# Kernel tuning notes

Hardware: AMD Instinct MI355X
Metric: run time of the kernel (lower is better)

## Reference

```python
import jax, jax.numpy as jnp
import numpy as np

H = 512

def _lstm_layer(x_tbd, W_ih, b, W_hh):
    # x_tbd: [T, B, D]; W_ih: [4H, D]; b: [4H]; W_hh: [4H, H]
    T, B, _ = x_tbd.shape
    # precompute input projections for all timesteps (same math, batched GEMM)
    xp = jnp.einsum('tbd,gd->tbg', x_tbd, W_ih) + b  # [T, B, 4H]

    def step(carry, xp_t):
        h, c = carry
        gates = xp_t + h @ W_hh.T  # [B, 4H]
        i, f, g, o = jnp.split(gates, 4, axis=-1)
        i = jax.nn.sigmoid(i)
        f = jax.nn.sigmoid(f)
        g = jnp.tanh(g)
        o = jax.nn.sigmoid(o)
        c_next = f * c + i * g
        h_next = o * jnp.tanh(c_next)
        return (h_next, c_next), h_next

    h0 = jnp.zeros((B, H), dtype=x_tbd.dtype)
    c0 = jnp.zeros((B, H), dtype=x_tbd.dtype)
    (h_n, c_n), hs = jax.lax.scan(step, (h0, c0), xp)
    return hs, h_n, c_n  # hs: [T, B, H]


def setup_inputs() -> dict:
    key = jax.random.key(0)
    ks = jax.random.split(key, 5)
    D = 256
    x = jax.random.normal(ks[0], (32, 1024, D), dtype=jnp.float32)
    s = 0.05
    W_ih0 = jax.random.normal(ks[1], (4 * H, D), dtype=jnp.float32) * s
    W_hh0 = jax.random.normal(ks[2], (4 * H, H), dtype=jnp.float32) * s
    W_ih1 = jax.random.normal(ks[3], (4 * H, H), dtype=jnp.float32) * s
    W_hh1 = jax.random.normal(ks[4], (4 * H, H), dtype=jnp.float32) * s
    # bias init: zeros, forget-gate slice [H:2H] = 1.0 (per _init_weights)
    b = jnp.zeros((4 * H,), dtype=jnp.float32).at[H:2 * H].set(1.0)
    return {"x": x, "W_ih0": W_ih0, "b0": b, "W_hh0": W_hh0,
            "W_ih1": W_ih1, "b1": b, "W_hh1": W_hh1}


def reference(x, W_ih0, b0, W_hh0, W_ih1, b1, W_hh1):
    # batch_first: [B, T, D] -> [T, B, D]
    x_tbd = jnp.transpose(x, (1, 0, 2))
    hs0, h0n, c0n = _lstm_layer(x_tbd, W_ih0, b0, W_hh0)
    hs1, h1n, c1n = _lstm_layer(hs0, W_ih1, b1, W_hh1)
    output = jnp.transpose(hs1, (1, 0, 2))  # [B, T, H]
    h_n = jnp.stack([h0n, h1n], axis=0)  # [num_layers, B, H]
    c_n = jnp.stack([c0n, c1n], axis=0)
    return output, h_n, c_n
```

## Files before the change

kernel.cpp:

```cpp
#include <hip/hip_runtime.h>


typedef __bf16 bf16x8 __attribute__((ext_vector_type(8)));
typedef float  f32x4  __attribute__((ext_vector_type(4)));
typedef float  f32x2  __attribute__((ext_vector_type(2)));
typedef unsigned long long u64;
typedef unsigned int u32;

#define MFMA16(a, b, c) __builtin_amdgcn_mfma_f32_16x16x32_bf16((a), (b), (c), 0, 0, 0)
#define SCOPE_AGENT __HIP_MEMORY_SCOPE_AGENT

__device__ __forceinline__ float fsigm(float x) { return 1.0f / (1.0f + __expf(-x)); }
__device__ __forceinline__ float ftanh(float x) {
    x = fminf(15.0f, fmaxf(-15.0f, x));
    float e = __expf(2.0f * x);
    return (e - 1.0f) / (e + 1.0f);
}

__device__ __forceinline__ bf16x8 frag_from(u64 lo, u64 hi) {
    union { u64 u[2]; bf16x8 v; } x;
    x.u[0] = lo; x.u[1] = hi;
    return x.v;
}

__global__ void pack_w3(const float* __restrict__ W0, const float* __restrict__ W1,
                        const float* __restrict__ W2, __bf16* __restrict__ O0,
                        __bf16* __restrict__ O1, __bf16* __restrict__ O2) {
    int gtid = blockIdx.x * 256 + threadIdx.x;
    int sel  = gtid >> 17;
    const float* W = (sel == 0) ? W0 : (sel == 1) ? W1 : W2;
    __bf16* WB     = (sel == 0) ? O0 : (sel == 1) ? O1 : O2;
    int tid  = gtid & 131071;
    int lane = tid & 63;
    int kk   = (tid >> 6) & 15;
    int v    = (tid >> 10) & 3;
    int w    = tid >> 12;
    int n    = v * 16 + (lane & 15);
    int grow = (n >> 4) * 512 + w * 16 + (n & 15);
    int k0   = kk * 32 + (lane >> 4) * 8;
    const float* src = W + (size_t)grow * 512 + k0;
    bf16x8 val;
#pragma unroll
    for (int e = 0; e < 8; e++) val[e] = (__bf16)src[e];
    *(bf16x8*)(WB + (size_t)tid * 8) = val;
}

__global__ __launch_bounds__(256, 2) void gemm_xp(const float* __restrict__ A,
                                                  const float* __restrict__ W,
                                                  __bf16* __restrict__ out, int K) {
    const int tid = threadIdx.x, lane = tid & 63, wv = tid >> 6;
    const int bm = blockIdx.x >> 4, bn = blockIdx.x & 15;
    const int m_base = bm * 128 + (wv & 1) * 64;
    const int n_base = bn * 128 + (wv >> 1) * 64;
    const int kq = (lane >> 4) * 8;
    const int rl = lane & 15;

    f32x4 acc[4][4];
#pragma unroll
    for (int i = 0; i < 4; i++)
#pragma unroll
        for (int j = 0; j < 4; j++) acc[i][j] = (f32x4){0.f, 0.f, 0.f, 0.f};

    const int nk = K >> 5;
    for (int kk = 0; kk < nk; kk++) {
        int k0 = kk * 32 + kq;
        bf16x8 af[4], bfr[4];
#pragma unroll
        for (int mt = 0; mt < 4; mt++) {
            int row = m_base + mt * 16 + rl;
            const float* ap = A + (size_t)((row & 31) * 1024 + (row >> 5)) * K + k0;
#pragma unroll
            for (int e = 0; e < 8; e++) af[mt][e] = (__bf16)ap[e];
        }
#pragma unroll
        for (int nt = 0; nt < 4; nt++) {
            int n = n_base + nt * 16 + rl;
            const float* wp = W + (size_t)n * K + k0;
#pragma unroll
            for (int e = 0; e < 8; e++) bfr[nt][e] = (__bf16)wp[e];
        }
#pragma unroll
        for (int mt = 0; mt < 4; mt++)
#pragma unroll
            for (int nt = 0; nt < 4; nt++)
                acc[mt][nt] = MFMA16(af[mt], bfr[nt], acc[mt][nt]);
    }

    const int rq = (lane >> 4) * 4;
#pragma unroll
    for (int mt = 0; mt < 4; mt++)
#pragma unroll
        for (int nt = 0; nt < 4; nt++)
#pragma unroll
            for (int r = 0; r < 4; r++) {
                int row = m_base + mt * 16 + rq + r;
                int col = n_base + nt * 16 + rl;
                out[(size_t)row * 2048 + col] = (__bf16)acc[mt][nt][r];
            }
}

__global__ __launch_bounds__(256, 1) void lstm_pipe3(
    const __bf16* __restrict__ xp0,
    const __bf16* __restrict__ WB0,
    const __bf16* __restrict__ WBw1,
    const __bf16* __restrict__ WBi1,
    const float* __restrict__ bias0,
    const float* __restrict__ bias1,
    __bf16* __restrict__ hbuf0,
    __bf16* __restrict__ hbuf1,
    __bf16* __restrict__ hs0s,
    __bf16* __restrict__ xp1r,
    float* __restrict__ out_f32,
    float* __restrict__ hn_out,
    float* __restrict__ cn_out,
    int* __restrict__ fL0,
    int* __restrict__ fX,
    int* __restrict__ fL1) {
    const int tid  = threadIdx.x;
    const int role = blockIdx.x >> 5;
    const int w    = blockIdx.x & 31;
    const int lane = tid & 63;
    const int wv   = tid >> 6;

    __shared__ __bf16 h_lds[32 * 516];
    __shared__ float  g_lds[32 * 68];

    bf16x8 wreg[16];
    {
        const __bf16* WB = (role == 0) ? WB0 : (role == 1) ? WBi1 : WBw1;
        const __bf16* wb = WB + (size_t)(w * 4 + wv) * 16 * 512 + lane * 8;
#pragma unroll
        for (int kk = 0; kk < 16; kk++) wreg[kk] = *(const bf16x8*)(wb + kk * 512);
    }

    const int b  = tid >> 3;
    const int jp = tid & 7;
    const int j0 = w * 16 + jp * 2;
    const int arow = lane & 15;
    const int kq8  = (lane >> 4) * 8;

    f32x2 bsv[4];
    if (role != 1) {
        const float* bias = (role == 0) ? bias0 : bias1;
#pragma unroll
        for (int g = 0; g < 4; g++) bsv[g] = *(const f32x2*)(bias + g * 512 + j0);
    }
    float cc0 = 0.f, cc1 = 0.f;

    __bf16* hbuf = (role == 0) ? hbuf0 : hbuf1;
    int* fMy = (role == 0) ? fL0 : (role == 1) ? fX : fL1;

    u32 xc[4] = {0, 0, 0, 0}, xn[4] = {0, 0, 0, 0};
    if (role == 0) {
#pragma unroll
        for (int g = 0; g < 4; g++)
            xc[g] = *(const u32*)(xp0 + (size_t)b * 2048 + g * 512 + j0);
    }

    for (int t = 0; t < 1024; t++) {
        if (role == 0) {
            int tn = (t < 1023) ? t + 1 : 1023;
#pragma unroll
            for (int g = 0; g < 4; g++)
                xn[g] = *(const u32*)(xp0 + (size_t)(tn * 32 + b) * 2048 + g * 512 + j0);
            if (t > 0) {
                if (tid < 32)
                    while (__hip_atomic_load(&fL0[tid * 1024 + t - 1], __ATOMIC_RELAXED,
                                             SCOPE_AGENT) == 0) {}
                asm volatile("" ::: "memory");
                __syncthreads();
            }
        } else if (role == 1) {
            if (tid < 32)
                while (__hip_atomic_load(&fL0[tid * 1024 + t], __ATOMIC_RELAXED,
                                         SCOPE_AGENT) == 0) {}
            else if (tid == 32 && t >= 4)
                while (__hip_atomic_load(&fL1[w * 1024 + t - 4], __ATOMIC_RELAXED,
                                         SCOPE_AGENT) == 0) {}
            asm volatile("" ::: "memory");
            __syncthreads();
        } else {
            if (tid < 32) {
                if (t > 0)
                    while (__hip_atomic_load(&fL1[tid * 1024 + t - 1], __ATOMIC_RELAXED,
                                             SCOPE_AGENT) == 0) {}
            } else if (tid == 32) {
                while (__hip_atomic_load(&fX[w * 1024 + t], __ATOMIC_RELAXED,
                                         SCOPE_AGENT) == 0) {}
            }
            asm volatile("" ::: "memory");
            __syncthreads();
        }

        u32 xpr[4];
        if (role == 2) {
            const __bf16* xs = xp1r + (size_t)(t & 3) * 65536 + (size_t)b * 2048 + j0;
#pragma unroll
            for (int g = 0; g < 4; g++)
                xpr[g] = __hip_atomic_load((const u32*)(xs + g * 512),
                                           __ATOMIC_RELAXED, SCOPE_AGENT);
        }
        {
            const u64* hg = (role == 1)
                ? (const u64*)(hs0s + (size_t)t * 16384)
                : (const u64*)(hbuf + (size_t)(t & 1) * 16384);
            u64 hv[16];
#pragma unroll
            for (int i = 0; i < 16; i++)
                hv[i] = __hip_atomic_load(hg + i * 256 + tid, __ATOMIC_RELAXED, SCOPE_AGENT);
#pragma unroll
            for (int i = 0; i < 16; i++) {
                int f  = (i * 256 + tid) * 4;
                int br = f >> 9, col = f & 511;
                *(u64*)(h_lds + br * 516 + col) = hv[i];
            }
        }
        __syncthreads();

        f32x4 acc0 = (f32x4){0.f, 0.f, 0.f, 0.f};
        f32x4 acc1 = (f32x4){0.f, 0.f, 0.f, 0.f};
#pragma unroll
        for (int kk = 0; kk < 16; kk++) {
            const __bf16* p0 = h_lds + arow * 516 + kq8 + kk * 32;
            const __bf16* p1 = p0 + 16 * 516;
            bf16x8 a0 = frag_from(*(const u64*)p0, *(const u64*)(p0 + 4));
            bf16x8 a1 = frag_from(*(const u64*)p1, *(const u64*)(p1 + 4));
            acc0 = MFMA16(a0, wreg[kk], acc0);
            acc1 = MFMA16(a1, wreg[kk], acc1);
        }
        {
            int col   = wv * 16 + (lane & 15);
            int rbase = (lane >> 4) * 4;
#pragma unroll
            for (int r = 0; r < 4; r++) {
                g_lds[(rbase + r) * 68 + col]      = acc0[r];
                g_lds[(16 + rbase + r) * 68 + col] = acc1[r];
            }
        }
        __syncthreads();

        if (role == 1) {
            const float* gl = g_lds + b * 68 + jp * 2;
            __bf16* xd = xp1r + (size_t)(t & 3) * 65536 + (size_t)b * 2048 + j0;
#pragma unroll
            for (int g = 0; g < 4; g++) {
                f32x2 gv = *(const f32x2*)(gl + g * 16);
                union { __bf16 v2[2]; u32 u; } pu;
                pu.v2[0] = (__bf16)gv[0]; pu.v2[1] = (__bf16)gv[1];
                __hip_atomic_store((u32*)(xd + g * 512), pu.u,
                                   __ATOMIC_RELAXED, SCOPE_AGENT);
            }
            asm volatile("s_waitcnt vmcnt(0)" ::: "memory");
            __syncthreads();
            if (tid == 0)
                __hip_atomic_store(&fX[w * 1024 + t], 1, __ATOMIC_RELAXED, SCOPE_AGENT);
        } else {
            float hf0, hf1;
            {
                u32 x0 = (role == 0) ? xc[0] : xpr[0];
                u32 x1 = (role == 0) ? xc[1] : xpr[1];
                u32 x2 = (role == 0) ? xc[2] : xpr[2];
                u32 x3 = (role == 0) ? xc[3] : xpr[3];
                union { u32 u; __bf16 v2[2]; } xi, xf, xg, xo;
                xi.u = x0; xf.u = x1; xg.u = x2; xo.u = x3;
                const float* gl = g_lds + b * 68 + jp * 2;
                f32x2 gi = *(const f32x2*)(gl);
                f32x2 gf = *(const f32x2*)(gl + 16);
                f32x2 gg = *(const f32x2*)(gl + 32);
                f32x2 go = *(const f32x2*)(gl + 48);

                float i0 = fsigm(gi[0] + (float)xi.v2[0] + bsv[0][0]);
                float f0 = fsigm(gf[0] + (float)xf.v2[0] + bsv[1][0]);
                float g0 = ftanh(gg[0] + (float)xg.v2[0] + bsv[2][0]);
                float o0 = fsigm(go[0] + (float)xo.v2[0] + bsv[3][0]);
                cc0 = f0 * cc0 + i0 * g0;
                hf0 = o0 * ftanh(cc0);

                float i1 = fsigm(gi[1] + (float)xi.v2[1] + bsv[0][1]);
                float f1 = fsigm(gf[1] + (float)xf.v2[1] + bsv[1][1]);
                float g1 = ftanh(gg[1] + (float)xg.v2[1] + bsv[2][1]);
                float o1 = fsigm(go[1] + (float)xo.v2[1] + bsv[3][1]);
                cc1 = f1 * cc1 + i1 * g1;
                hf1 = o1 * ftanh(cc1);
            }
            union { __bf16 v2[2]; u32 u; } hu;
            hu.v2[0] = (__bf16)hf0; hu.v2[1] = (__bf16)hf1;

            __hip_atomic_store((u32*)(hbuf + (size_t)((t + 1) & 1) * 16384 +
                                      (size_t)b * 512 + j0),
                               hu.u, __ATOMIC_RELAXED, SCOPE_AGENT);
            if (role == 0)
                __hip_atomic_store((u32*)(hs0s + ((size_t)t * 32 + b) * 512 + j0), hu.u,
                                   __ATOMIC_RELAXED, SCOPE_AGENT);
            asm volatile("s_waitcnt vmcnt(0)" ::: "memory");
            __syncthreads();
            if (tid == 0)
                __hip_atomic_store(&fMy[w * 1024 + t], 1, __ATOMIC_RELAXED, SCOPE_AGENT);

            if (role == 2)
                *(f32x2*)(out_f32 + (size_t)b * 524288 + (size_t)t * 512 + j0) =
                    (f32x2){hf0, hf1};
            if (t == 1023) {
                int li = (role == 0) ? 0 : 1;
                *(f32x2*)(hn_out + (size_t)li * 16384 + (size_t)b * 512 + j0) =
                    (f32x2){hf0, hf1};
                *(f32x2*)(cn_out + (size_t)li * 16384 + (size_t)b * 512 + j0) =
                    (f32x2){cc0, cc1};
            }
#pragma unroll
            for (int g = 0; g < 4; g++) xc[g] = xn[g];
        }
    }
}

extern "C" void kernel_launch(void* const* d_in, const int* in_sizes, int n_in,
                              void* d_out, int out_size, void* d_ws, size_t ws_size,
                              hipStream_t stream) {
    (void)in_sizes; (void)n_in; (void)out_size; (void)ws_size;
    const float* x    = (const float*)d_in[0];
    const float* Wih0 = (const float*)d_in[1];
    const float* b0   = (const float*)d_in[2];
    const float* Whh0 = (const float*)d_in[3];
    const float* Wih1 = (const float*)d_in[4];
    const float* b1   = (const float*)d_in[5];
    const float* Whh1 = (const float*)d_in[6];
    float* dout = (float*)d_out;

    char* wsb = (char*)d_ws;
    int*    fL0   = (int*)wsb;
    int*    fX    = (int*)(wsb + (128 << 10));
    int*    fL1   = (int*)(wsb + (256 << 10));
    __bf16* hbuf0 = (__bf16*)(wsb + (384 << 10));
    __bf16* hbuf1 = (__bf16*)(wsb + (448 << 10));
    __bf16* WB0   = (__bf16*)(wsb + (512 << 10));
    __bf16* WBw1  = (__bf16*)(wsb + (512 << 10) + (2 << 20));
    __bf16* WBi1  = (__bf16*)(wsb + (512 << 10) + (4 << 20));
    __bf16* xp1r  = (__bf16*)(wsb + (512 << 10) + (6 << 20));
    __bf16* hs0s  = (__bf16*)(wsb + (1 << 20) + (7 << 20));
    __bf16* xpb   = (__bf16*)(wsb + (40 << 20));

    (void)hipMemsetAsync(wsb, 0, 512 << 10, stream);

    pack_w3<<<dim3(1536), dim3(256), 0, stream>>>(Whh0, Whh1, Wih1, WB0, WBw1, WBi1);

    gemm_xp<<<dim3(4096), dim3(256), 0, stream>>>(x, Wih0, xpb, 256);

    lstm_pipe3<<<dim3(96), dim3(256), 0, stream>>>(
        xpb, WB0, WBw1, WBi1, b0, b1, hbuf0, hbuf1, hs0s, xp1r,
        dout, dout + 16777216, dout + 16777216 + 32768, fL0, fX, fL1);
}
```

Baseline: 3.869 ms.

## Embed phase tags in recurrent h buffers to replace flag-based step sync

The recurrent hidden-state exchange now stores each bf16 pair alongside a 32-bit phase tag in a 64-bit word. Consumers poll the data directly until every tag matches the expected phase, instead of waiting on per-block flags. This removes the store-drain wait, barrier and flag write from the critical path of layer 0's and layer 1's recurrences. In exchange, the h buffers double in size, every poll reads twice as many bytes, and readers spin on the payload itself. Layer 1 now signals its flag (used for throttling the xp1 ring) at step start rather than after writing h.

Result: slower. 4.030 ms (+4.2%).

```diff
diff --git a/kernel.cpp b/kernel.cpp
--- a/kernel.cpp
+++ b/kernel.cpp
@@ -21,6 +21,26 @@
     union { u64 u[2]; bf16x8 v; } x;
     x.u[0] = lo; x.u[1] = hi;
     return x.v;
+}
+
+__device__ __forceinline__ void poll_pairs16(const u64* __restrict__ base, int tid,
+                                             u32 ph, u64* hv) {
+    u64 q0[16], q1[16];
+    u32 bad;
+    do {
+#pragma unroll
+        for (int i = 0; i < 16; i++) {
+            int f = i * 256 + tid;
+            q0[i] = __hip_atomic_load(base + 2 * f,     __ATOMIC_RELAXED, SCOPE_AGENT);
+            q1[i] = __hip_atomic_load(base + 2 * f + 1, __ATOMIC_RELAXED, SCOPE_AGENT);
+        }
+        bad = 0;
+#pragma unroll
+        for (int i = 0; i < 16; i++)
+            bad |= ((u32)(q0[i] >> 32) ^ ph) | ((u32)(q1[i] >> 32) ^ ph);
+    } while (bad != 0);
+#pragma unroll
+    for (int i = 0; i < 16; i++) hv[i] = (q0[i] & 0xFFFFFFFFull) | (q1[i] << 32);
 }
 
 __global__ void pack_w3(const float* __restrict__ W0, const float* __restrict__ W1,
@@ -106,8 +126,8 @@
     const __bf16* __restrict__ WBi1,
     const float* __restrict__ bias0,
     const float* __restrict__ bias1,
-    __bf16* __restrict__ hbuf0,
-    __bf16* __restrict__ hbuf1,
+    u64* __restrict__ hbuf0,
+    u64* __restrict__ hbuf1,
     __bf16* __restrict__ hs0s,
     __bf16* __restrict__ xp1r,
     float* __restrict__ out_f32,
@@ -136,6 +156,7 @@
     const int b  = tid >> 3;
     const int jp = tid & 7;
     const int j0 = w * 16 + jp * 2;
+    const int pi = b * 256 + w * 8 + jp;
     const int arow = lane & 15;
     const int kq8  = (lane >> 4) * 8;
 
@@ -147,8 +168,7 @@
     }
     float cc0 = 0.f, cc1 = 0.f;
 
-    __bf16* hbuf = (role == 0) ? hbuf0 : hbuf1;
-    int* fMy = (role == 0) ? fL0 : (role == 1) ? fX : fL1;
+    u64* hbuf = (role == 0) ? hbuf0 : hbuf1;
 
     u32 xc[4] = {0, 0, 0, 0}, xn[4] = {0, 0, 0, 0};
     if (role == 0) {
@@ -158,17 +178,19 @@
     }
 
     for (int t = 0; t < 1024; t++) {
+        u64 hv[16];
+        u32 xpr[4];
+
         if (role == 0) {
             int tn = (t < 1023) ? t + 1 : 1023;
 #pragma unroll
             for (int g = 0; g < 4; g++)
                 xn[g] = *(const u32*)(xp0 + (size_t)(tn * 32 + b) * 2048 + g * 512 + j0);
             if (t > 0) {
-                if (tid < 32)
-                    while (__hip_atomic_load(&fL0[tid * 1024 + t - 1], __ATOMIC_RELAXED,
-                                             SCOPE_AGENT) == 0) {}
-                asm volatile("" ::: "memory");
-                __syncthreads();
+                poll_pairs16(hbuf0 + (size_t)(t & 1) * 8192, tid, (u32)(t >> 1) + 1, hv);
+            } else {
+#pragma unroll
+                for (int i = 0; i < 16; i++) hv[i] = 0;
             }
         } else if (role == 1) {
             if (tid < 32)
@@ -179,43 +201,40 @@
                                          SCOPE_AGENT) == 0) {}
             asm volatile("" ::: "memory");
             __syncthreads();
+            const u64* hg = (const u64*)(hs0s + (size_t)t * 16384);
+#pragma unroll
+            for (int i = 0; i < 16; i++)
+                hv[i] = __hip_atomic_load(hg + i * 256 + tid, __ATOMIC_RELAXED, SCOPE_AGENT);
         } else {
-            if (tid < 32) {
-                if (t > 0)
-                    while (__hip_atomic_load(&fL1[tid * 1024 + t - 1], __ATOMIC_RELAXED,
-                                             SCOPE_AGENT) == 0) {}
-            } else if (tid == 32) {
+            if (tid == 32)
                 while (__hip_atomic_load(&fX[w * 1024 + t], __ATOMIC_RELAXED,
                                          SCOPE_AGENT) == 0) {}
-            }
             asm volatile("" ::: "memory");
             __syncthreads();
-        }
-
-        u32 xpr[4];
-        if (role == 2) {
             const __bf16* xs = xp1r + (size_t)(t & 3) * 65536 + (size_t)b * 2048 + j0;
 #pragma unroll
             for (int g = 0; g < 4; g++)
                 xpr[g] = __hip_atomic_load((const u32*)(xs + g * 512),
                                            __ATOMIC_RELAXED, SCOPE_AGENT);
-        }
-        {
-            const u64* hg = (role == 1)
-                ? (const u64*)(hs0s + (size_t)t * 16384)
-                : (const u64*)(hbuf + (size_t)(t & 1) * 16384);
-            u64 hv[16];
-#pragma unroll
-            for (int i = 0; i < 16; i++)
-                hv[i] = __hip_atomic_load(hg + i * 256 + tid, __ATOMIC_RELAXED, SCOPE_AGENT);
-#pragma unroll
-            for (int i = 0; i < 16; i++) {
-                int f  = (i * 256 + tid) * 4;
-                int br = f >> 9, col = f & 511;
-                *(u64*)(h_lds + br * 516 + col) = hv[i];
-            }
-        }
+            if (t > 0) {
+                poll_pairs16(hbuf1 + (size_t)(t & 1) * 8192, tid, (u32)(t >> 1) + 1, hv);
+            } else {
+#pragma unroll
+                for (int i = 0; i < 16; i++) hv[i] = 0;
+            }
+        }
+
+#pragma unroll
+        for (int i = 0; i < 16; i++) {
+            int f  = (i * 256 + tid) * 4;
+            int br = f >> 9, col = f & 511;
+            *(u64*)(h_lds + br * 516 + col) = hv[i];
+        }
+        if (role == 2)
+            asm volatile("s_waitcnt vmcnt(0)" ::: "memory");
         __syncthreads();
+        if (role == 2 && tid == 0)
+            __hip_atomic_store(&fL1[w * 1024 + t], 1, __ATOMIC_RELAXED, SCOPE_AGENT);
 
         f32x4 acc0 = (f32x4){0.f, 0.f, 0.f, 0.f};
         f32x4 acc1 = (f32x4){0.f, 0.f, 0.f, 0.f};
@@ -286,20 +305,21 @@
             union { __bf16 v2[2]; u32 u; } hu;
             hu.v2[0] = (__bf16)hf0; hu.v2[1] = (__bf16)hf1;
 
-            __hip_atomic_store((u32*)(hbuf + (size_t)((t + 1) & 1) * 16384 +
-                                      (size_t)b * 512 + j0),
-                               hu.u, __ATOMIC_RELAXED, SCOPE_AGENT);
-            if (role == 0)
+            u64 hp = (u64)hu.u | ((u64)((u32)((t + 1) >> 1) + 1) << 32);
+            __hip_atomic_store(hbuf + (size_t)((t + 1) & 1) * 8192 + pi, hp,
+                               __ATOMIC_RELAXED, SCOPE_AGENT);
+
+            if (role == 0) {
                 __hip_atomic_store((u32*)(hs0s + ((size_t)t * 32 + b) * 512 + j0), hu.u,
                                    __ATOMIC_RELAXED, SCOPE_AGENT);
-            asm volatile("s_waitcnt vmcnt(0)" ::: "memory");
-            __syncthreads();
-            if (tid == 0)
-                __hip_atomic_store(&fMy[w * 1024 + t], 1, __ATOMIC_RELAXED, SCOPE_AGENT);
-
-            if (role == 2)
+                asm volatile("s_waitcnt vmcnt(0)" ::: "memory");
+                __syncthreads();
+                if (tid == 0)
+                    __hip_atomic_store(&fL0[w * 1024 + t], 1, __ATOMIC_RELAXED, SCOPE_AGENT);
+            } else {
                 *(f32x2*)(out_f32 + (size_t)b * 524288 + (size_t)t * 512 + j0) =
                     (f32x2){hf0, hf1};
+            }
             if (t == 1023) {
                 int li = (role == 0) ? 0 : 1;
                 *(f32x2*)(hn_out + (size_t)li * 16384 + (size_t)b * 512 + j0) =
@@ -330,16 +350,16 @@
     int*    fL0   = (int*)wsb;
     int*    fX    = (int*)(wsb + (128 << 10));
     int*    fL1   = (int*)(wsb + (256 << 10));
-    __bf16* hbuf0 = (__bf16*)(wsb + (384 << 10));
-    __bf16* hbuf1 = (__bf16*)(wsb + (448 << 10));
-    __bf16* WB0   = (__bf16*)(wsb + (512 << 10));
-    __bf16* WBw1  = (__bf16*)(wsb + (512 << 10) + (2 << 20));
-    __bf16* WBi1  = (__bf16*)(wsb + (512 << 10) + (4 << 20));
-    __bf16* xp1r  = (__bf16*)(wsb + (512 << 10) + (6 << 20));
-    __bf16* hs0s  = (__bf16*)(wsb + (1 << 20) + (7 << 20));
+    u64*    hbuf0 = (u64*)(wsb + (384 << 10));
+    u64*    hbuf1 = (u64*)(wsb + (512 << 10));
+    __bf16* WB0   = (__bf16*)(wsb + (640 << 10));
+    __bf16* WBw1  = (__bf16*)(wsb + (640 << 10) + (2 << 20));
+    __bf16* WBi1  = (__bf16*)(wsb + (640 << 10) + (4 << 20));
+    __bf16* xp1r  = (__bf16*)(wsb + (640 << 10) + (6 << 20));
+    __bf16* hs0s  = (__bf16*)(wsb + (8 << 20));
     __bf16* xpb   = (__bf16*)(wsb + (40 << 20));
 
-    (void)hipMemsetAsync(wsb, 0, 512 << 10, stream);
+    (void)hipMemsetAsync(wsb, 0, 640 << 10, stream);
 
     pack_w3<<<dim3(1536), dim3(256), 0, stream>>>(Whh0, Whh1, Wih1, WB0, WBw1, WBi1);
 
```

## Fuse input-projection GEMM into LSTM kernel with per-timestep readiness counters

Applied to the files above, without the earlier changes.

Removes the separate gemm_xp launch and runs the layer-0 input projection on 512 extra worker blocks inside the recurrent kernel. Each worker stores bf16 pairs with atomic stores and bumps a per-row-block counter, and the layer-0 recurrence blocks spin on that counter before loading the next timestep's projection. This lets the recurrence start before the whole GEMM finishes. In exchange it adds a spin wait and a barrier on every step, and it relies on all 608 blocks being resident at once.

Measured after the change: 3.715 ms. 4.0% less time.

```diff
diff --git a/kernel.cpp b/kernel.cpp
--- a/kernel.cpp
+++ b/kernel.cpp
@@ -45,62 +45,10 @@
     *(bf16x8*)(WB + (size_t)tid * 8) = val;
 }
 
-__global__ __launch_bounds__(256, 2) void gemm_xp(const float* __restrict__ A,
-                                                  const float* __restrict__ W,
-                                                  __bf16* __restrict__ out, int K) {
-    const int tid = threadIdx.x, lane = tid & 63, wv = tid >> 6;
-    const int bm = blockIdx.x >> 4, bn = blockIdx.x & 15;
-    const int m_base = bm * 128 + (wv & 1) * 64;
-    const int n_base = bn * 128 + (wv >> 1) * 64;
-    const int kq = (lane >> 4) * 8;
-    const int rl = lane & 15;
-
-    f32x4 acc[4][4];
-#pragma unroll
-    for (int i = 0; i < 4; i++)
-#pragma unroll
-        for (int j = 0; j < 4; j++) acc[i][j] = (f32x4){0.f, 0.f, 0.f, 0.f};
-
-    const int nk = K >> 5;
-    for (int kk = 0; kk < nk; kk++) {
-        int k0 = kk * 32 + kq;
-        bf16x8 af[4], bfr[4];
-#pragma unroll
-        for (int mt = 0; mt < 4; mt++) {
-            int row = m_base + mt * 16 + rl;
-            const float* ap = A + (size_t)((row & 31) * 1024 + (row >> 5)) * K + k0;
-#pragma unroll
-            for (int e = 0; e < 8; e++) af[mt][e] = (__bf16)ap[e];
-        }
-#pragma unroll
-        for (int nt = 0; nt < 4; nt++) {
-            int n = n_base + nt * 16 + rl;
-            const float* wp = W + (size_t)n * K + k0;
-#pragma unroll
-            for (int e = 0; e < 8; e++) bfr[nt][e] = (__bf16)wp[e];
-        }
-#pragma unroll
-        for (int mt = 0; mt < 4; mt++)
-#pragma unroll
-            for (int nt = 0; nt < 4; nt++)
-                acc[mt][nt] = MFMA16(af[mt], bfr[nt], acc[mt][nt]);
-    }
-
-    const int rq = (lane >> 4) * 4;
-#pragma unroll
-    for (int mt = 0; mt < 4; mt++)
-#pragma unroll
-        for (int nt = 0; nt < 4; nt++)
-#pragma unroll
-            for (int r = 0; r < 4; r++) {
-                int row = m_base + mt * 16 + rq + r;
-                int col = n_base + nt * 16 + rl;
-                out[(size_t)row * 2048 + col] = (__bf16)acc[mt][nt][r];
-            }
-}
-
-__global__ __launch_bounds__(256, 1) void lstm_pipe3(
-    const __bf16* __restrict__ xp0,
+__global__ __launch_bounds__(256, 1) void lstm_fused(
+    const float* __restrict__ x,
+    const float* __restrict__ Wih0,
+    __bf16* __restrict__ xp0,
     const __bf16* __restrict__ WB0,
     const __bf16* __restrict__ WBw1,
     const __bf16* __restrict__ WBi1,
@@ -115,12 +63,82 @@
     float* __restrict__ cn_out,
     int* __restrict__ fL0,
     int* __restrict__ fX,
-    int* __restrict__ fL1) {
+    int* __restrict__ fL1,
+    u32* __restrict__ xpcnt) {
     const int tid  = threadIdx.x;
+    const int lane = tid & 63;
+    const int wv   = tid >> 6;
+
+    if (blockIdx.x >= 96) {
+        const int wkr = blockIdx.x - 96;
+        const int kq = (lane >> 4) * 8;
+        const int rl = lane & 15;
+        const int rq = (lane >> 4) * 4;
+#pragma unroll 1
+        for (int it = 0; it < 8; it++) {
+            const int tile = wkr + 512 * it;
+            const int bm = tile >> 4, bn = tile & 15;
+            const int m_base = bm * 128 + (wv & 1) * 64;
+            const int n_base = bn * 128 + (wv >> 1) * 64;
+
+            f32x4 acc[4][4];
+#pragma unroll
+            for (int i = 0; i < 4; i++)
+#pragma unroll
+                for (int j = 0; j < 4; j++) acc[i][j] = (f32x4){0.f, 0.f, 0.f, 0.f};
+
+#pragma unroll 1
+            for (int kk = 0; kk < 8; kk++) {
+                int k0 = kk * 32 + kq;
+                bf16x8 af[4], bfr[4];
+#pragma unroll
+                for (int mt = 0; mt < 4; mt++) {
+                    int row = m_base + mt * 16 + rl;
+                    const float* ap = x + (size_t)((row & 31) * 1024 + (row >> 5)) * 256 + k0;
+#pragma unroll
+                    for (int e = 0; e < 8; e++) af[mt][e] = (__bf16)ap[e];
+                }
+#pragma unroll
+                for (int nt = 0; nt < 4; nt++) {
+                    int n = n_base + nt * 16 + rl;
+                    const float* wp = Wih0 + (size_t)n * 256 + k0;
+#pragma unroll
+                    for (int e = 0; e < 8; e++) bfr[nt][e] = (__bf16)wp[e];
+                }
+#pragma unroll
+                for (int mt = 0; mt < 4; mt++)
+#pragma unroll
+                    for (int nt = 0; nt < 4; nt++)
+                        acc[mt][nt] = MFMA16(af[mt], bfr[nt], acc[mt][nt]);
+            }
+
+#pragma unroll
+            for (int mt = 0; mt < 4; mt++)
+#pragma unroll
+                for (int nt = 0; nt < 4; nt++)
+#pragma unroll
+                    for (int r = 0; r < 4; r++) {
+                        float v  = acc[mt][nt][r];
+                        float vn = __shfl_down(v, 1);
+                        if (!(rl & 1)) {
+                            int row = m_base + mt * 16 + rq + r;
+                            int col = n_base + nt * 16 + rl;
+                            union { __bf16 v2[2]; u32 u; } pu;
+                            pu.v2[0] = (__bf16)v; pu.v2[1] = (__bf16)vn;
+                            __hip_atomic_store((u32*)(xp0 + (size_t)row * 2048 + col),
+                                               pu.u, __ATOMIC_RELAXED, SCOPE_AGENT);
+                        }
+                    }
+            asm volatile("s_waitcnt vmcnt(0)" ::: "memory");
+            __syncthreads();
+            if (tid == 0)
+                __hip_atomic_fetch_add(&xpcnt[bm], 1u, __ATOMIC_RELAXED, SCOPE_AGENT);
+        }
+        return;
+    }
+
     const int role = blockIdx.x >> 5;
     const int w    = blockIdx.x & 31;
-    const int lane = tid & 63;
-    const int wv   = tid >> 6;
 
     __shared__ __bf16 h_lds[32 * 516];
     __shared__ float  g_lds[32 * 68];
@@ -152,24 +170,34 @@
 
     u32 xc[4] = {0, 0, 0, 0}, xn[4] = {0, 0, 0, 0};
     if (role == 0) {
+        if (tid == 32)
+            while (__hip_atomic_load(&xpcnt[0], __ATOMIC_RELAXED, SCOPE_AGENT) < 16u) {}
+        asm volatile("" ::: "memory");
+        __syncthreads();
 #pragma unroll
         for (int g = 0; g < 4; g++)
-            xc[g] = *(const u32*)(xp0 + (size_t)b * 2048 + g * 512 + j0);
+            xc[g] = __hip_atomic_load((const u32*)(xp0 + (size_t)b * 2048 + g * 512 + j0),
+                                      __ATOMIC_RELAXED, SCOPE_AGENT);
     }
 
     for (int t = 0; t < 1024; t++) {
         if (role == 0) {
             int tn = (t < 1023) ? t + 1 : 1023;
-#pragma unroll
-            for (int g = 0; g < 4; g++)
-                xn[g] = *(const u32*)(xp0 + (size_t)(tn * 32 + b) * 2048 + g * 512 + j0);
             if (t > 0) {
                 if (tid < 32)
                     while (__hip_atomic_load(&fL0[tid * 1024 + t - 1], __ATOMIC_RELAXED,
                                              SCOPE_AGENT) == 0) {}
-                asm volatile("" ::: "memory");
-                __syncthreads();
-            }
+            }
+            if (tid == 32)
+                while (__hip_atomic_load(&xpcnt[tn >> 2], __ATOMIC_RELAXED,
+                                         SCOPE_AGENT) < 16u) {}
+            asm volatile("" ::: "memory");
+            __syncthreads();
+#pragma unroll
+            for (int g = 0; g < 4; g++)
+                xn[g] = __hip_atomic_load(
+                    (const u32*)(xp0 + (size_t)(tn * 32 + b) * 2048 + g * 512 + j0),
+                    __ATOMIC_RELAXED, SCOPE_AGENT);
         } else if (role == 1) {
             if (tid < 32)
                 while (__hip_atomic_load(&fL0[tid * 1024 + t], __ATOMIC_RELAXED,
@@ -332,20 +360,19 @@
     int*    fL1   = (int*)(wsb + (256 << 10));
     __bf16* hbuf0 = (__bf16*)(wsb + (384 << 10));
     __bf16* hbuf1 = (__bf16*)(wsb + (448 << 10));
-    __bf16* WB0   = (__bf16*)(wsb + (512 << 10));
-    __bf16* WBw1  = (__bf16*)(wsb + (512 << 10) + (2 << 20));
-    __bf16* WBi1  = (__bf16*)(wsb + (512 << 10) + (4 << 20));
-    __bf16* xp1r  = (__bf16*)(wsb + (512 << 10) + (6 << 20));
-    __bf16* hs0s  = (__bf16*)(wsb + (1 << 20) + (7 << 20));
+    u32*    xpcnt = (u32*)(wsb + (512 << 10));
+    __bf16* WB0   = (__bf16*)(wsb + (516 << 10));
+    __bf16* WBw1  = (__bf16*)(wsb + (516 << 10) + (2 << 20));
+    __bf16* WBi1  = (__bf16*)(wsb + (516 << 10) + (4 << 20));
+    __bf16* xp1r  = (__bf16*)(wsb + (516 << 10) + (6 << 20));
+    __bf16* hs0s  = (__bf16*)(wsb + (8 << 20));
     __bf16* xpb   = (__bf16*)(wsb + (40 << 20));
 
-    (void)hipMemsetAsync(wsb, 0, 512 << 10, stream);
+    (void)hipMemsetAsync(wsb, 0, 516 << 10, stream);
 
     pack_w3<<<dim3(1536), dim3(256), 0, stream>>>(Whh0, Whh1, Wih1, WB0, WBw1, WBi1);
 
-    gemm_xp<<<dim3(4096), dim3(256), 0, stream>>>(x, Wih0, xpb, 256);
-
-    lstm_pipe3<<<dim3(96), dim3(256), 0, stream>>>(
-        xpb, WB0, WBw1, WBi1, b0, b1, hbuf0, hbuf1, hs0s, xp1r,
-        dout, dout + 16777216, dout + 16777216 + 32768, fL0, fX, fL1);
-}
+    lstm_fused<<<dim3(608), dim3(256), 0, stream>>>(
+        x, Wih0, xpb, WB0, WBw1, WBi1, b0, b1, hbuf0, hbuf1, hs0s, xp1r,
+        dout, dout + 16777216, dout + 16777216 + 32768, fL0, fX, fL1, xpcnt);
+}
```
